# Optimization experiments

Measured on AMD Instinct MI355X. Metric: run time of the kernel, lower is better.

Reference implementation:

```python
import math
import jax, jax.numpy as jnp
import numpy as np

N_HEAD = 16
DIM = 1024
HEAD_DIM = DIM // N_HEAD  # 64


def _rope(x):
    # x: [b, h, t, d] ; lucidrains RotaryEmbedding default: interleaved pairs,
    # inv_freq = 1/theta^(2i/d), theta=10000, positions = arange(t)
    t, d = x.shape[2], x.shape[3]
    inv_freq = 1.0 / (10000.0 ** (jnp.arange(0, d, 2, dtype=jnp.float32) / d))  # [d/2]
    freqs = jnp.arange(t, dtype=jnp.float32)[:, None] * inv_freq[None, :]       # [t, d/2]
    emb = jnp.repeat(freqs, 2, axis=-1)                                          # [t, d]
    cos = jnp.cos(emb).astype(x.dtype)
    sin = jnp.sin(emb).astype(x.dtype)
    x1 = x[..., ::2]
    x2 = x[..., 1::2]
    rot = jnp.stack([-x2, x1], axis=-1).reshape(x.shape)  # rotate_half (interleaved)
    return x * cos + rot * sin


def setup_inputs() -> dict:
    key = jax.random.key(0)
    k1, k2, k3 = jax.random.split(key, 3)
    b, t = 2, 2048
    x = jax.random.normal(k1, (b, t, DIM), dtype=jnp.float32)
    w_qkv = jax.random.normal(k2, (DIM, 3 * DIM), dtype=jnp.float32) * (1.0 / math.sqrt(DIM))
    b_qkv = jnp.zeros((3 * DIM,), dtype=jnp.float32)
    w_out = jax.random.normal(k3, (DIM, DIM), dtype=jnp.float32) * (1.0 / math.sqrt(DIM))
    b_out = jnp.zeros((DIM,), dtype=jnp.float32)
    return {"x": x, "w_qkv": w_qkv, "b_qkv": b_qkv, "w_out": w_out, "b_out": b_out}


def reference(x, w_qkv, b_qkv, w_out, b_out):
    b, t, d = x.shape
    qkv = jnp.einsum('btd,de->bte', x, w_qkv) + b_qkv  # [b,t,3d]
    q, k, v = jnp.split(qkv, 3, axis=-1)
    # [b,t,d] -> [b,h,t,nd]
    def heads(z):
        return z.reshape(b, t, N_HEAD, HEAD_DIM).transpose(0, 2, 1, 3)
    q, k, v = heads(q), heads(k), heads(v)
    q = _rope(q)
    k = _rope(k)
    attn = jnp.einsum('bhqd,bhkd->bhqk', q, k) / math.sqrt(HEAD_DIM)
    attn = jax.nn.softmax(attn, axis=-1)
    # dropout is identity in eval mode
    out = jnp.einsum('bhqk,bhkd->bhqd', attn, v)
    out = out.transpose(0, 2, 1, 3).reshape(b, t, d)
    return jnp.einsum('btd,de->bte', out, w_out) + b_out
```

## Files before the change

kernel.cpp:

```cpp
#include <hip/hip_runtime.h>
#include <hip/hip_bf16.h>

typedef unsigned short u16;
typedef unsigned int u32;
typedef __attribute__((ext_vector_type(8))) short bf16x8;
typedef __attribute__((ext_vector_type(4))) float f32x4;
typedef __attribute__((ext_vector_type(16))) float f32x16;

typedef __attribute__((address_space(1))) const u32* gas_ptr;
typedef __attribute__((address_space(3))) u32* las_ptr;

__device__ __forceinline__ void gld16(const void* g, void* l) {
  __builtin_amdgcn_global_load_lds((gas_ptr)g, (las_ptr)l, 16, 0, 0);
}

__device__ __forceinline__ u16 f2bf(float f) {
  unsigned u = __float_as_uint(f);
  u = u + 0x7fffu + ((u >> 16) & 1u);
  return (u16)(u >> 16);
}

__global__ __launch_bounds__(256) void prep(const float* __restrict__ x, u16* __restrict__ x_bf,
                                            const float* __restrict__ wqkv, u16* __restrict__ wqkvT,
                                            const float* __restrict__ wout, u16* __restrict__ woutT,
                                            float2* __restrict__ cs) {
  __shared__ float tile[32][33];
  const int b = blockIdx.x, tid = threadIdx.x;
  if (b < 4096) {
    int i = b * 256 + tid;
    float4 v = reinterpret_cast<const float4*>(x)[i];
    ushort4 o = make_ushort4(f2bf(v.x), f2bf(v.y), f2bf(v.z), f2bf(v.w));
    reinterpret_cast<ushort4*>(x_bf)[i] = o;
  } else if (b < 8192) {
    const float* in; u16* out; int R, C, bx, by;
    if (b < 7168) { in = wqkv; out = wqkvT; R = 1024; C = 3072; int b2 = b - 4096; bx = b2 % 96; by = b2 / 96; }
    else          { in = wout; out = woutT; R = 1024; C = 1024; int b3 = b - 7168; bx = b3 % 32; by = b3 / 32; }
    int tx = tid & 31, ty = tid >> 5;
    int c0 = bx * 32, r0 = by * 32;
#pragma unroll
    for (int i = 0; i < 32; i += 8)
      tile[ty + i][tx] = in[(size_t)(r0 + ty + i) * C + c0 + tx];
    __syncthreads();
#pragma unroll
    for (int i = 0; i < 32; i += 8)
      out[(size_t)(c0 + ty + i) * R + r0 + tx] = f2bf(tile[tx][ty + i]);
  } else {
    int idx = (b - 8192) * 256 + tid;
    int i = idx & 31, t = idx >> 5;
    float invf = powf(10000.0f, -(float)(2 * i) / 64.0f);
    float f = (float)t * invf;
    cs[idx] = make_float2(cosf(f), sinf(f));
  }
}

#define BM 128
#define BN 128
#define BKK 32
__global__ __launch_bounds__(256) void gemm_bt(
    const u16* __restrict__ A, const u16* __restrict__ Bt, const float* __restrict__ bias,
    float* __restrict__ Cf, u16* __restrict__ q_ws, u16* __restrict__ k_ws, u16* __restrict__ v_ws,
    const float2* __restrict__ cs, int M, int N, int K, int mode) {
  __shared__ u16 As[BM][BKK];
  __shared__ u16 Bs[BN][BKK];
  const int tid = threadIdx.x;
  const int lane = tid & 63;
  const int wid = tid >> 6;
  const int wr = wid >> 1, wc = wid & 1;
  const int fr = lane & 15, fg = lane >> 4;
  const int m0 = blockIdx.y * BM, n0 = blockIdx.x * BN;

  const int row_l = lane >> 2;
  const int slot_l = lane & 3;

  f32x4 acc[4][4] = {};

  for (int k0 = 0; k0 < K; k0 += BKK) {
#pragma unroll
    for (int i = 0; i < 2; i++) {
      int rowA = wid * 32 + i * 16;
      gld16(A  + (size_t)(m0 + rowA + row_l) * K + k0 + slot_l * 8, &As[rowA][0]);
      gld16(Bt + (size_t)(n0 + rowA + row_l) * K + k0 + slot_l * 8, &Bs[rowA][0]);
    }
    __syncthreads();
    bf16x8 af[4], bfr[4];
#pragma unroll
    for (int i = 0; i < 4; i++)
      af[i] = *reinterpret_cast<const bf16x8*>(&As[wr * 64 + i * 16 + fr][fg * 8]);
#pragma unroll
    for (int j = 0; j < 4; j++)
      bfr[j] = *reinterpret_cast<const bf16x8*>(&Bs[wc * 64 + j * 16 + fr][fg * 8]);
#pragma unroll
    for (int i = 0; i < 4; i++)
#pragma unroll
      for (int j = 0; j < 4; j++)
        acc[i][j] = __builtin_amdgcn_mfma_f32_16x16x32_bf16(af[i], bfr[j], acc[i][j], 0, 0, 0);
    __syncthreads();
  }

#pragma unroll
  for (int i = 0; i < 4; i++) {
    int rowb = m0 + wr * 64 + i * 16 + fg * 4;
#pragma unroll
    for (int j = 0; j < 4; j++) {
      int col = n0 + wc * 64 + j * 16 + fr;
      float bv = bias[col];
      if (mode == 0) {
#pragma unroll
        for (int r = 0; r < 4; r++)
          Cf[(size_t)(rowb + r) * N + col] = acc[i][j][r] + bv;
      } else {
        int bb = rowb >> 11, t0 = rowb & 2047;
        int sec = col >> 10, nn = col & 1023;
        int h = nn >> 6, d = nn & 63;
        int bh = (bb << 4) + h;
        if (sec == 2) {
          ushort4 st;
          st.x = f2bf(acc[i][j][0] + bv);
          st.y = f2bf(acc[i][j][1] + bv);
          st.z = f2bf(acc[i][j][2] + bv);
          st.w = f2bf(acc[i][j][3] + bv);
          *reinterpret_cast<ushort4*>(v_ws + ((size_t)(bh * 64 + d)) * 2048 + t0) = st;
        } else {
          u16* dst = (sec == 0) ? q_ws : k_ws;
#pragma unroll
          for (int r = 0; r < 4; r++) {
            float v = acc[i][j][r] + bv;
            float vp = __shfl_xor(v, 1);
            int t = t0 + r;
            float2 c_s = cs[(t << 5) + (d >> 1)];
            float vv = (d & 1) ? fmaf(v, c_s.x, vp * c_s.y) : fmaf(v, c_s.x, -vp * c_s.y);
            dst[((size_t)bh * 2048 + t) * 64 + d] = f2bf(vv);
          }
        }
      }
    }
  }
}

#define KVB 64
#define NT 32
#define CSC 0.18033688011112042f
#define THRL2 11.5415603f

__global__ __launch_bounds__(256, 2) void attn_fwd(const u16* __restrict__ q_ws,
                                                   const u16* __restrict__ k_ws,
                                                   const u16* __restrict__ v_ws,
                                                   u16* __restrict__ attn_out) {
  __shared__ u16 Klds[2][4096];
  __shared__ u16 Vlds[2][4096];

  const int tid = threadIdx.x, lane = tid & 63, w = tid >> 6;
  const int l31 = lane & 31, hi = lane >> 5;
  const int bid = blockIdx.x;
  const int wrk = (bid & 7) * 64 + (bid >> 3);
  const int bh = wrk >> 4;
  const int q0 = (wrk & 15) * 128 + w * 32;
  const size_t base = (size_t)bh * (2048 * 64);

  bf16x8 qf[4];
#pragma unroll
  for (int db = 0; db < 4; db++)
    qf[db] = *reinterpret_cast<const bf16x8*>(
        q_ws + base + (size_t)(q0 + l31) * 64 + db * 16 + hi * 8);

  f32x16 Oa[2] = {};
  float m_i = -1e30f, l_i = 0.f;

  const int krow_l = lane >> 3, kslot_l = lane & 7;
  const u16* kg = k_ws + base;
  const u16* vgT = v_ws + base;

#define STAGE_K(kv, buf)                                                          \
  {                                                                               \
    _Pragma("unroll") for (int i = 0; i < 2; i++) {                               \
      int row = w * 16 + i * 8 + krow_l;                                          \
      int srcslot = kslot_l ^ (row & 7);                                          \
      gld16(kg + (size_t)((kv) + row) * 64 + srcslot * 8, &Klds[buf][(w * 16 + i * 8) * 64]); \
    }                                                                             \
  }
#define STAGE_V(kv, buf)                                                          \
  {                                                                               \
    _Pragma("unroll") for (int i = 0; i < 2; i++) {                               \
      int row = w * 16 + i * 8 + krow_l;                             \
      int srcslot = kslot_l ^ (row & 7);                                          \
      gld16(vgT + (size_t)row * 2048 + (kv) + srcslot * 8, &Vlds[buf][(w * 16 + i * 8) * 64]); \
    }                                                                             \
  }

  STAGE_K(0, 0);
  STAGE_V(0, 0);
  __syncthreads();

  int cur = 0;
  for (int t = 0; t < NT; t++) {
    if (t + 1 < NT) {
      STAGE_K((t + 1) * KVB, cur ^ 1);
      STAGE_V((t + 1) * KVB, cur ^ 1);
    }

    const char* Kb = (const char*)&Klds[cur][0];
    const char* Vb = (const char*)&Vlds[cur][0];

    bf16x8 kf[2][4];
#pragma unroll
    for (int ks = 0; ks < 2; ks++) {
      int krow = (l31 + 32 * ks) * 128;
      int ksw = (l31 & 7) << 4;
#pragma unroll
      for (int db = 0; db < 4; db++)
        kf[ks][db] = *reinterpret_cast<const bf16x8*>(Kb + krow + ((db * 32 + hi * 16) ^ ksw));
    }

    f32x16 s0 = {}, s1 = {};
    __builtin_amdgcn_s_setprio(1);
#pragma unroll
    for (int db = 0; db < 4; db++) {
      s0 = __builtin_amdgcn_mfma_f32_32x32x16_bf16(kf[0][db], qf[db], s0, 0, 0, 0);
      s1 = __builtin_amdgcn_mfma_f32_32x32x16_bf16(kf[1][db], qf[db], s1, 0, 0, 0);
    }
    __builtin_amdgcn_s_setprio(0);

    float a[8];
#pragma unroll
    for (int i = 0; i < 8; i++)
      a[i] = fmaxf(fmaxf(s0[i], s0[i + 8]), fmaxf(s1[i], s1[i + 8]));
    a[0] = fmaxf(a[0], a[4]); a[1] = fmaxf(a[1], a[5]);
    a[2] = fmaxf(a[2], a[6]); a[3] = fmaxf(a[3], a[7]);
    float zx = fmaxf(fmaxf(a[0], a[1]), fmaxf(a[2], a[3])) * CSC;
    zx = fmaxf(zx, __shfl_xor(zx, 32));

    if (__any(zx > m_i + THRL2)) {
      float mn = fmaxf(m_i, zx);
      float alpha = exp2f(m_i - mn);
      m_i = mn;
      l_i *= alpha;
#pragma unroll
      for (int ds = 0; ds < 2; ds++)
#pragma unroll
        for (int r = 0; r < 16; r++) Oa[ds][r] *= alpha;
    }

    float p[32];
#pragma unroll
    for (int i = 0; i < 16; i++) {
      p[i]      = exp2f(fmaf(s0[i], CSC, -m_i));
      p[16 + i] = exp2f(fmaf(s1[i], CSC, -m_i));
    }
    float r0 = 0.f, r1 = 0.f, r2 = 0.f, r3 = 0.f;
#pragma unroll
    for (int i = 0; i < 8; i++) {
      r0 += p[i]; r1 += p[i + 8]; r2 += p[i + 16]; r3 += p[i + 24];
    }
    float rs = (r0 + r1) + (r2 + r3);
    rs += __shfl_xor(rs, 32);
    l_i += rs;

    u32 pw[16];
#pragma unroll
    for (int kk = 0; kk < 2; kk++)
#pragma unroll
      for (int wd = 0; wd < 8; wd++) {
        __hip_bfloat162 hh =
            __float22bfloat162_rn(make_float2(p[kk * 16 + 2 * wd], p[kk * 16 + 2 * wd + 1]));
        u32 uu;
        __builtin_memcpy(&uu, &hh, 4);
        pw[kk * 8 + wd] = uu;
      }

    int vsw = (l31 & 7) << 4;
    __builtin_amdgcn_s_setprio(1);
#pragma unroll
    for (int ds = 0; ds < 2; ds++) {
      int vrow = (l31 + 32 * ds) * 128;
#pragma unroll
      for (int kb = 0; kb < 4; kb++) {
        uint2 va = *(const uint2*)(Vb + vrow + ((kb * 32 + hi * 8) ^ vsw));
        uint2 vb2 = *(const uint2*)(Vb + vrow + ((kb * 32 + hi * 8 + 16) ^ vsw));
        union { u32 u[4]; bf16x8 v; } vf, pf;
        vf.u[0] = va.x; vf.u[1] = va.y; vf.u[2] = vb2.x; vf.u[3] = vb2.y;
        int pb = (kb >> 1) * 8 + (kb & 1) * 4;
        pf.u[0] = pw[pb]; pf.u[1] = pw[pb + 1]; pf.u[2] = pw[pb + 2]; pf.u[3] = pw[pb + 3];
        Oa[ds] = __builtin_amdgcn_mfma_f32_32x32x16_bf16(vf.v, pf.v, Oa[ds], 0, 0, 0);
      }
    }
    __builtin_amdgcn_s_setprio(0);

    __syncthreads();
    cur ^= 1;
  }

  const int b = bh >> 4, h = bh & 15;
  float invl = 1.0f / l_i;
  int row = q0 + l31;
  size_t rbase = ((size_t)(b * 2048 + row)) * 1024 + h * 64;
#pragma unroll
  for (int ds = 0; ds < 2; ds++)
#pragma unroll
    for (int rg = 0; rg < 4; rg++) {
      int d0 = rg * 8 + hi * 4 + ds * 32;
      ushort4 st;
      st.x = f2bf(Oa[ds][rg * 4 + 0] * invl);
      st.y = f2bf(Oa[ds][rg * 4 + 1] * invl);
      st.z = f2bf(Oa[ds][rg * 4 + 2] * invl);
      st.w = f2bf(Oa[ds][rg * 4 + 3] * invl);
      *reinterpret_cast<ushort4*>(attn_out + rbase + d0) = st;
    }
#undef STAGE_K
#undef STAGE_V
}

extern "C" void kernel_launch(void* const* d_in, const int* in_sizes, int n_in,
                              void* d_out, int out_size, void* d_ws, size_t ws_size,
                              hipStream_t stream) {
  const float* x     = (const float*)d_in[0];
  const float* w_qkv = (const float*)d_in[1];
  const float* b_qkv = (const float*)d_in[2];
  const float* w_out = (const float*)d_in[3];
  const float* b_out = (const float*)d_in[4];
  float* out = (float*)d_out;

  char* ws = (char*)d_ws;
  const size_t MB = 1024 * 1024;
  u16*    x_bf   = (u16*)(ws);
  u16*    wqkvT  = (u16*)(ws + 8 * MB);
  u16*    woutT  = (u16*)(ws + 14 * MB);
  u16*    q_ws   = (u16*)(ws + 16 * MB);
  u16*    k_ws   = (u16*)(ws + 24 * MB);
  u16*    v_ws   = (u16*)(ws + 32 * MB);
  u16*    attn_o = (u16*)(ws + 40 * MB);
  float2* cs     = (float2*)(ws + 48 * MB);

  prep<<<8448, 256, 0, stream>>>(x, x_bf, w_qkv, wqkvT, w_out, woutT, cs);
  gemm_bt<<<dim3(24, 32), 256, 0, stream>>>(x_bf, wqkvT, b_qkv, nullptr, q_ws, k_ws, v_ws,
                                            cs, 4096, 3072, 1024, 1);
  attn_fwd<<<512, 256, 0, stream>>>(q_ws, k_ws, v_ws, attn_o);
  gemm_bt<<<dim3(8, 32), 256, 0, stream>>>(attn_o, woutT, b_out, out, nullptr, nullptr, nullptr,
                                           nullptr, 4096, 1024, 1024, 0);
}
```

Measured before the change: 249.6 us.

## Split attention KV range in two with merge kernel, MFMA row sums, narrower out-proj tiles

Attention now splits each query tile's KV range into two halves, doubling the grid to 1024 blocks with higher occupancy. Each half writes unnormalized bf16 partial outputs plus (max, sum) to scratch, and a new merge kernel combines them. Row sums are computed with an MFMA against a ones vector instead of scalar adds and shuffles. The output projection GEMM is templated to use 64-wide N tiles, doubling its block count. The split adds an extra kernel launch, extra memory traffic for the partials, and bf16 rounding of the unnormalized partials.

Result: slower. 272.6 us (+9.2%).

```diff
diff --git a/kernel.cpp b/kernel.cpp
--- a/kernel.cpp
+++ b/kernel.cpp
@@ -18,6 +18,9 @@
   unsigned u = __float_as_uint(f);
   u = u + 0x7fffu + ((u >> 16) & 1u);
   return (u16)(u >> 16);
+}
+__device__ __forceinline__ float bf2f(u16 h) {
+  return __uint_as_float(((unsigned)h) << 16);
 }
 
 __global__ __launch_bounds__(256) void prep(const float* __restrict__ x, u16* __restrict__ x_bf,
@@ -53,46 +56,50 @@
   }
 }
 
-#define BM 128
-#define BN 128
 #define BKK 32
+template <int BNT, int MODE>
 __global__ __launch_bounds__(256) void gemm_bt(
     const u16* __restrict__ A, const u16* __restrict__ Bt, const float* __restrict__ bias,
     float* __restrict__ Cf, u16* __restrict__ q_ws, u16* __restrict__ k_ws, u16* __restrict__ v_ws,
-    const float2* __restrict__ cs, int M, int N, int K, int mode) {
-  __shared__ u16 As[BM][BKK];
-  __shared__ u16 Bs[BN][BKK];
+    const float2* __restrict__ cs, int M, int N, int K) {
+  constexpr int NJ = BNT / 32;
+  __shared__ u16 As[128][BKK];
+  __shared__ u16 Bs[BNT][BKK];
   const int tid = threadIdx.x;
   const int lane = tid & 63;
   const int wid = tid >> 6;
   const int wr = wid >> 1, wc = wid & 1;
   const int fr = lane & 15, fg = lane >> 4;
-  const int m0 = blockIdx.y * BM, n0 = blockIdx.x * BN;
+  const int m0 = blockIdx.y * 128, n0 = blockIdx.x * BNT;
 
   const int row_l = lane >> 2;
   const int slot_l = lane & 3;
 
-  f32x4 acc[4][4] = {};
+  f32x4 acc[4][NJ] = {};
 
   for (int k0 = 0; k0 < K; k0 += BKK) {
 #pragma unroll
     for (int i = 0; i < 2; i++) {
       int rowA = wid * 32 + i * 16;
-      gld16(A  + (size_t)(m0 + rowA + row_l) * K + k0 + slot_l * 8, &As[rowA][0]);
-      gld16(Bt + (size_t)(n0 + rowA + row_l) * K + k0 + slot_l * 8, &Bs[rowA][0]);
+      gld16(A + (size_t)(m0 + rowA + row_l) * K + k0 + slot_l * 8, &As[rowA][0]);
+    }
+#pragma unroll
+    for (int i = 0; i < BNT / 64; i++) {
+      int rowB = wid * (BNT / 4) + i * 16;
+      gld16(Bt + (size_t)(n0 + rowB + row_l) * K + k0 + slot_l * 8, &Bs[rowB][0]);
     }
     __syncthreads();
-    bf16x8 af[4], bfr[4];
+    bf16x8 af[4], bfr[NJ];
 #pragma unroll
     for (int i = 0; i < 4; i++)
       af[i] = *reinterpret_cast<const bf16x8*>(&As[wr * 64 + i * 16 + fr][fg * 8]);
 #pragma unroll
-    for (int j = 0; j < 4; j++)
-      bfr[j] = *reinterpret_cast<const bf16x8*>(&Bs[wc * 64 + j * 16 + fr][fg * 8]);
+    for (int j = 0; j < NJ; j++)
+      bfr[j] = *reinterpret_cast<const bf16x8*>(&Bs[wc * (BNT / 2) + j * 16 + fr][fg * 8]);
 #pragma unroll
     for (int i = 0; i < 4; i++)
 #pragma unroll
-      for (int j = 0; j < 4; j++)
+      for (int j = 0; j < NJ; j++)
         acc[i][j] = __builtin_amdgcn_mfma_f32_16x16x32_bf16(af[i], bfr[j], acc[i][j], 0, 0, 0);
     __syncthreads();
   }
@@ -101,10 +108,10 @@
   for (int i = 0; i < 4; i++) {
     int rowb = m0 + wr * 64 + i * 16 + fg * 4;
 #pragma unroll
-    for (int j = 0; j < 4; j++) {
-      int col = n0 + wc * 64 + j * 16 + fr;
+    for (int j = 0; j < NJ; j++) {
+      int col = n0 + wc * (BNT / 2) + j * 16 + fr;
       float bv = bias[col];
-      if (mode == 0) {
+      if (MODE == 0) {
 #pragma unroll
         for (int r = 0; r < 4; r++)
           Cf[(size_t)(rowb + r) * N + col] = acc[i][j][r] + bv;
@@ -138,23 +145,27 @@
 }
 
 #define KVB 64
-#define NT 32
+#define NT 16
 #define CSC 0.18033688011112042f
 #define THRL2 11.5415603f
 
-__global__ __launch_bounds__(256, 2) void attn_fwd(const u16* __restrict__ q_ws,
+__global__ __launch_bounds__(256, 4) void attn_fwd(const u16* __restrict__ q_ws,
                                                    const u16* __restrict__ k_ws,
                                                    const u16* __restrict__ v_ws,
-                                                   u16* __restrict__ attn_out) {
+                                                   u16* __restrict__ pO,
+                                                   float2* __restrict__ pML) {
   __shared__ u16 Klds[2][4096];
   __shared__ u16 Vlds[2][4096];
 
   const int tid = threadIdx.x, lane = tid & 63, w = tid >> 6;
   const int l31 = lane & 31, hi = lane >> 5;
   const int bid = blockIdx.x;
-  const int wrk = (bid & 7) * 64 + (bid >> 3);
-  const int bh = wrk >> 4;
-  const int q0 = (wrk & 15) * 128 + w * 32;
+  const int wrk = (bid & 7) * 128 + (bid >> 3);
+  const int bh = wrk >> 5;
+  const int qt = (wrk >> 1) & 15;
+  const int kh = wrk & 1;
+  const int q0 = qt * 128 + w * 32;
+  const int kv0 = kh * 1024;
   const size_t base = (size_t)bh * (2048 * 64);
 
   bf16x8 qf[4];
@@ -163,8 +174,13 @@
     qf[db] = *reinterpret_cast<const bf16x8*>(
         q_ws + base + (size_t)(q0 + l31) * 64 + db * 16 + hi * 8);
 
+  bf16x8 onesv;
+#pragma unroll
+  for (int i = 0; i < 8; i++) onesv[i] = (short)0x3F80;
+
   f32x16 Oa[2] = {};
-  float m_i = -1e30f, l_i = 0.f;
+  f32x16 l_acc = {};
+  float m_i = -1e30f;
 
   const int krow_l = lane >> 3, kslot_l = lane & 7;
   const u16* kg = k_ws + base;
@@ -175,7 +191,7 @@
     _Pragma("unroll") for (int i = 0; i < 2; i++) {                               \
       int row = w * 16 + i * 8 + krow_l;                                          \
       int srcslot = kslot_l ^ (row & 7);                                          \
-      gld16(kg + (size_t)((kv) + row) * 64 + srcslot * 8, &Klds[buf][(w * 16 + i * 8) * 64]); \
+      gld16(kg + (size_t)(kv0 + (kv) + row) * 64 + srcslot * 8, &Klds[buf][(w * 16 + i * 8) * 64]); \
     }                                                                             \
   }
 #define STAGE_V(kv, buf)                                                          \
@@ -183,7 +199,7 @@
     _Pragma("unroll") for (int i = 0; i < 2; i++) {                               \
       int row = w * 16 + i * 8 + krow_l;                             \
       int srcslot = kslot_l ^ (row & 7);                                          \
-      gld16(vgT + (size_t)row * 2048 + (kv) + srcslot * 8, &Vlds[buf][(w * 16 + i * 8) * 64]); \
+      gld16(vgT + (size_t)row * 2048 + kv0 + (kv) + srcslot * 8, &Vlds[buf][(w * 16 + i * 8) * 64]); \
     }                                                                             \
   }
 
@@ -220,20 +236,20 @@
     }
     __builtin_amdgcn_s_setprio(0);
 
-    float a[8];
-#pragma unroll
-    for (int i = 0; i < 8; i++)
-      a[i] = fmaxf(fmaxf(s0[i], s0[i + 8]), fmaxf(s1[i], s1[i + 8]));
-    a[0] = fmaxf(a[0], a[4]); a[1] = fmaxf(a[1], a[5]);
-    a[2] = fmaxf(a[2], a[6]); a[3] = fmaxf(a[3], a[7]);
-    float zx = fmaxf(fmaxf(a[0], a[1]), fmaxf(a[2], a[3])) * CSC;
+    float zm0 = fmaxf(s0[0], s0[1]);
+#pragma unroll
+    for (int i = 2; i < 16; i += 2) zm0 = fmaxf(fmaxf(zm0, s0[i]), s0[i + 1]);
+    float zm1 = fmaxf(s1[0], s1[1]);
+#pragma unroll
+    for (int i = 2; i < 16; i += 2) zm1 = fmaxf(fmaxf(zm1, s1[i]), s1[i + 1]);
+    float zx = fmaxf(zm0, zm1) * CSC;
     zx = fmaxf(zx, __shfl_xor(zx, 32));
 
     if (__any(zx > m_i + THRL2)) {
       float mn = fmaxf(m_i, zx);
       float alpha = exp2f(m_i - mn);
       m_i = mn;
-      l_i *= alpha;
+      l_acc[0] *= alpha;
 #pragma unroll
       for (int ds = 0; ds < 2; ds++)
 #pragma unroll
@@ -246,29 +262,23 @@
       p[i]      = exp2f(fmaf(s0[i], CSC, -m_i));
       p[16 + i] = exp2f(fmaf(s1[i], CSC, -m_i));
     }
-    float r0 = 0.f, r1 = 0.f, r2 = 0.f, r3 = 0.f;
-#pragma unroll
-    for (int i = 0; i < 8; i++) {
-      r0 += p[i]; r1 += p[i + 8]; r2 += p[i + 16]; r3 += p[i + 24];
-    }
-    float rs = (r0 + r1) + (r2 + r3);
-    rs += __shfl_xor(rs, 32);
-    l_i += rs;
-
-    u32 pw[16];
+
+    union U4 { u32 u[4]; bf16x8 v; };
+    U4 pf[4];
 #pragma unroll
     for (int kk = 0; kk < 2; kk++)
 #pragma unroll
       for (int wd = 0; wd < 8; wd++) {
-        __hip_bfloat162 hh =
-            __float22bfloat162_rn(make_float2(p[kk * 16 + 2 * wd], p[kk * 16 + 2 * wd + 1]));
-        u32 uu;
-        __builtin_memcpy(&uu, &hh, 4);
-        pw[kk * 8 + wd] = uu;
+        u32 word = ((u32)f2bf(p[kk * 16 + 2 * wd + 1]) << 16) | (u32)f2bf(p[kk * 16 + 2 * wd]);
+        pf[kk * 2 + (wd >> 2)].u[wd & 3] = word;
       }
 
+    __builtin_amdgcn_s_setprio(1);
+#pragma unroll
+    for (int kb = 0; kb < 4; kb++)
+      l_acc = __builtin_amdgcn_mfma_f32_32x32x16_bf16(onesv, pf[kb].v, l_acc, 0, 0, 0);
+
     int vsw = (l31 & 7) << 4;
-    __builtin_amdgcn_s_setprio(1);
 #pragma unroll
     for (int ds = 0; ds < 2; ds++) {
       int vrow = (l31 + 32 * ds) * 128;
@@ -276,11 +286,9 @@
       for (int kb = 0; kb < 4; kb++) {
         uint2 va = *(const uint2*)(Vb + vrow + ((kb * 32 + hi * 8) ^ vsw));
         uint2 vb2 = *(const uint2*)(Vb + vrow + ((kb * 32 + hi * 8 + 16) ^ vsw));
-        union { u32 u[4]; bf16x8 v; } vf, pf;
+        U4 vf;
         vf.u[0] = va.x; vf.u[1] = va.y; vf.u[2] = vb2.x; vf.u[3] = vb2.y;
-        int pb = (kb >> 1) * 8 + (kb & 1) * 4;
-        pf.u[0] = pw[pb]; pf.u[1] = pw[pb + 1]; pf.u[2] = pw[pb + 2]; pf.u[3] = pw[pb + 3];
-        Oa[ds] = __builtin_amdgcn_mfma_f32_32x32x16_bf16(vf.v, pf.v, Oa[ds], 0, 0, 0);
+        Oa[ds] = __builtin_amdgcn_mfma_f32_32x32x16_bf16(vf.v, pf[kb].v, Oa[ds], 0, 0, 0);
       }
     }
     __builtin_amdgcn_s_setprio(0);
@@ -289,24 +297,51 @@
     cur ^= 1;
   }
 
-  const int b = bh >> 4, h = bh & 15;
-  float invl = 1.0f / l_i;
-  int row = q0 + l31;
-  size_t rbase = ((size_t)(b * 2048 + row)) * 1024 + h * 64;
+  const size_t prow = ((size_t)bh * 2048 + q0 + l31) * 2 + kh;
 #pragma unroll
   for (int ds = 0; ds < 2; ds++)
 #pragma unroll
     for (int rg = 0; rg < 4; rg++) {
       int d0 = rg * 8 + hi * 4 + ds * 32;
       ushort4 st;
-      st.x = f2bf(Oa[ds][rg * 4 + 0] * invl);
-      st.y = f2bf(Oa[ds][rg * 4 + 1] * invl);
-      st.z = f2bf(Oa[ds][rg * 4 + 2] * invl);
-      st.w = f2bf(Oa[ds][rg * 4 + 3] * invl);
-      *reinterpret_cast<ushort4*>(attn_out + rbase + d0) = st;
-    }
+      st.x = f2bf(Oa[ds][rg * 4 + 0]);
+      st.y = f2bf(Oa[ds][rg * 4 + 1]);
+      st.z = f2bf(Oa[ds][rg * 4 + 2]);
+      st.w = f2bf(Oa[ds][rg * 4 + 3]);
+      *reinterpret_cast<ushort4*>(pO + prow * 64 + d0) = st;
+    }
+  if (hi == 0) pML[prow] = make_float2(m_i, l_acc[0]);
 #undef STAGE_K
 #undef STAGE_V
+}
+
+__global__ __launch_bounds__(256) void attn_merge(const u16* __restrict__ pO,
+                                                  const float2* __restrict__ pML,
+                                                  u16* __restrict__ attn_o) {
+  int tid = blockIdx.x * 256 + threadIdx.x;
+  int row = tid >> 2, dq = (tid & 3) * 16;
+  float2 ml0 = pML[row * 2], ml1 = pML[row * 2 + 1];
+  float m = fmaxf(ml0.x, ml1.x);
+  float w0 = exp2f(ml0.x - m), w1 = exp2f(ml1.x - m);
+  float inv = 1.0f / (fmaf(ml0.y, w0, ml1.y * w1));
+  w0 *= inv; w1 *= inv;
+  const u16* o0 = pO + (size_t)row * 128 + dq;
+  const u16* o1 = o0 + 64;
+  int bh = row >> 11, q = row & 2047;
+  int b = bh >> 4, h = bh & 15;
+  u16* dst = attn_o + ((size_t)(b * 2048 + q)) * 1024 + h * 64 + dq;
+#pragma unroll
+  for (int c = 0; c < 2; c++) {
+    uint4 va = *reinterpret_cast<const uint4*>(o0 + c * 8);
+    uint4 vb = *reinterpret_cast<const uint4*>(o1 + c * 8);
+    union { u16 s[8]; uint4 v; } res;
+    const u16* pa = (const u16*)&va;
+    const u16* pb = (const u16*)&vb;
+#pragma unroll
+    for (int j = 0; j < 8; j++)
+      res.s[j] = f2bf(fmaf(bf2f(pa[j]), w0, bf2f(pb[j]) * w1));
+    *reinterpret_cast<uint4*>(dst + c * 8) = res.v;
+  }
 }
 
 extern "C" void kernel_launch(void* const* d_in, const int* in_sizes, int n_in,
@@ -321,19 +356,23 @@
 
   char* ws = (char*)d_ws;
   const size_t MB = 1024 * 1024;
+  u16*    pO     = (u16*)(ws);
   u16*    x_bf   = (u16*)(ws);
   u16*    wqkvT  = (u16*)(ws + 8 * MB);
-  u16*    woutT  = (u16*)(ws + 14 * MB);
-  u16*    q_ws   = (u16*)(ws + 16 * MB);
-  u16*    k_ws   = (u16*)(ws + 24 * MB);
-  u16*    v_ws   = (u16*)(ws + 32 * MB);
-  u16*    attn_o = (u16*)(ws + 40 * MB);
+  u16*    q_ws   = (u16*)(ws + 14 * MB);
+  u16*    k_ws   = (u16*)(ws + 22 * MB);
+  u16*    v_ws   = (u16*)(ws + 30 * MB);
+  u16*    attn_o = (u16*)(ws + 38 * MB);
+  u16*    woutT  = (u16*)(ws + 46 * MB);
   float2* cs     = (float2*)(ws + 48 * MB);
+  float2* pML    = (float2*)(ws + 48 * MB + 512 * 1024);
 
   prep<<<8448, 256, 0, stream>>>(x, x_bf, w_qkv, wqkvT, w_out, woutT, cs);
-  gemm_bt<<<dim3(24, 32), 256, 0, stream>>>(x_bf, wqkvT, b_qkv, nullptr, q_ws, k_ws, v_ws,
-                                            cs, 4096, 3072, 1024, 1);
-  attn_fwd<<<512, 256, 0, stream>>>(q_ws, k_ws, v_ws, attn_o);
-  gemm_bt<<<dim3(8, 32), 256, 0, stream>>>(attn_o, woutT, b_out, out, nullptr, nullptr, nullptr,
-                                           nullptr, 4096, 1024, 1024, 0);
-}
+  gemm_bt<128, 1><<<dim3(24, 32), 256, 0, stream>>>(x_bf, wqkvT, b_qkv, nullptr,
+                                                    q_ws, k_ws, v_ws, cs, 4096, 3072, 1024);
+  attn_fwd<<<1024, 256, 0, stream>>>(q_ws, k_ws, v_ws, pO, pML);
+  attn_merge<<<1024, 256, 0, stream>>>(pO, pML, attn_o);
+  gemm_bt<64, 0><<<dim3(16, 32), 256, 0, stream>>>(attn_o, woutT, b_out, out,
+                                                   nullptr, nullptr, nullptr, nullptr,
+                                                   4096, 1024, 1024);
+}
```
